# Kernel optimization log

Hardware: AMD Instinct MI355X
Metric: run time of the kernel (lower is better)

## Reference

```python
import jax, jax.numpy as jnp
import numpy as np
import math

N = 100000   # nodes
E = 500000   # edges
IN_C = 128
EDGE_D = 64
HEADS = 4
OUT_C = 32
HC = HEADS * OUT_C  # 128


def setup_inputs() -> dict:
    key = jax.random.key(0)
    ks = jax.random.split(key, 12)
    s_in = 1.0 / math.sqrt(IN_C)
    s_e = 1.0 / math.sqrt(EDGE_D)
    return {
        "x": jax.random.normal(ks[0], (N, IN_C), jnp.float32),
        "edge_index": jax.random.randint(ks[1], (2, E), 0, N, dtype=jnp.int32),
        "edge_attr": jax.random.normal(ks[2], (E, EDGE_D), jnp.float32),
        "Wq": jax.random.uniform(ks[3], (HC, IN_C), jnp.float32, -s_in, s_in),
        "bq": jax.random.uniform(ks[4], (HC,), jnp.float32, -s_in, s_in),
        "Wk": jax.random.uniform(ks[5], (HC, IN_C), jnp.float32, -s_in, s_in),
        "bk": jax.random.uniform(ks[6], (HC,), jnp.float32, -s_in, s_in),
        "Wv": jax.random.uniform(ks[7], (HC, IN_C), jnp.float32, -s_in, s_in),
        "bv": jax.random.uniform(ks[8], (HC,), jnp.float32, -s_in, s_in),
        "We": jax.random.uniform(ks[9], (HC, EDGE_D), jnp.float32, -s_e, s_e),
        "Ws": jax.random.uniform(ks[10], (HC, IN_C), jnp.float32, -s_in, s_in),
        "bs": jax.random.uniform(ks[11], (HC,), jnp.float32, -s_in, s_in),
    }


def reference(x, edge_index, edge_attr, Wq, bq, Wk, bk, Wv, bv, We, Ws, bs):
    src = edge_index[0]
    dst = edge_index[1]
    x_i = x[dst]                       # [E, IN_C] target-node feats
    x_j = x[src]                       # [E, IN_C] source-node feats

    e = (edge_attr @ We.T).reshape(E, HEADS, OUT_C)
    q = (x_i @ Wq.T + bq).reshape(E, HEADS, OUT_C)
    k = (x_j @ Wk.T + bk).reshape(E, HEADS, OUT_C) + e

    alpha = jnp.sum(q * k, axis=-1) / jnp.sqrt(jnp.float32(OUT_C))  # [E, H]
    # Faithful to the source: GLOBAL per-column max (not per-segment), then
    # segment-sum of exponentials over destination nodes.
    m = jnp.max(alpha, axis=0)                                      # [H]
    exp_a = jnp.exp(alpha - m)                                      # [E, H]
    denom = jax.ops.segment_sum(exp_a, dst, num_segments=N)         # [N, H]
    alpha = exp_a / (denom[dst] + 1e-16)                            # [E, H]

    v = (x_j @ Wv.T + bv).reshape(E, HEADS, OUT_C) + e
    msg = v * alpha[:, :, None]                                     # [E, H, C]

    out = jax.ops.segment_sum(msg.reshape(E, HC), dst, num_segments=N)  # [N, HC]
    out = out + (x @ Ws.T + bs)
    return out
```

## Files before the change

kernel.cpp:

```cpp
#include <hip/hip_runtime.h>
#include <hip/hip_bf16.h>
#include <math.h>

#define N_NODES 100000
#define N_EDGES 500000
#define M0 8.0f
#define INV_SQRT32 0.17677669529663687f

#define NB_HIST 977
#define NB_PROJ 1563
#define NB_EE   3907
#define GRID_MEGA (NB_HIST + NB_PROJ + NB_EE)

typedef __attribute__((ext_vector_type(8))) short bf16x8;
typedef __attribute__((ext_vector_type(4))) float f32x4;
typedef __attribute__((ext_vector_type(8))) unsigned short us8;

static __device__ __forceinline__ unsigned short f2bf(float f) {
    __hip_bfloat16 h = __float2bfloat16(f);
    return *(unsigned short*)&h;
}

static __device__ __forceinline__ void split4(float4 v, ushort4& hv, ushort4& lv) {
    const unsigned short h0 = f2bf(v.x), h1 = f2bf(v.y),
                         h2 = f2bf(v.z), h3 = f2bf(v.w);
    hv.x = h0; hv.y = h1; hv.z = h2; hv.w = h3;
    lv.x = f2bf(v.x - __uint_as_float((unsigned)h0 << 16));
    lv.y = f2bf(v.y - __uint_as_float((unsigned)h1 << 16));
    lv.z = f2bf(v.z - __uint_as_float((unsigned)h2 << 16));
    lv.w = f2bf(v.w - __uint_as_float((unsigned)h3 << 16));
}

__global__ __launch_bounds__(256) void prep_kernel(
    const float* __restrict__ Wq, const float* __restrict__ Wk,
    const float* __restrict__ Wv, const float* __restrict__ Ws,
    const float* __restrict__ We,
    unsigned short* __restrict__ WBh, unsigned short* __restrict__ WBl,
    unsigned short* __restrict__ WEh, unsigned short* __restrict__ WEl,
    int* __restrict__ cursor)
{
    const int i = blockIdx.x * 256 + threadIdx.x;
    if (i < N_NODES) cursor[i] = 0;
    if (i < 65536) {
        const int p = i >> 14;
        const float* W = (p == 0) ? Wq : (p == 1) ? Wk : (p == 2) ? Wv : Ws;
        const float v = W[i & 16383];
        const unsigned short h = f2bf(v);
        WBh[i] = h;
        WBl[i] = f2bf(v - __uint_as_float((unsigned)h << 16));
    } else if (i < 73728) {
        const int idx = i - 65536;
        const float v = We[idx];
        const unsigned short h = f2bf(v);
        WEh[idx] = h;
        WEl[idx] = f2bf(v - __uint_as_float((unsigned)h << 16));
    }
}

__global__ __launch_bounds__(512, 4) void mega_kernel(
    const float* __restrict__ x, const int* __restrict__ ei,
    const float* __restrict__ ea,
    const unsigned short* __restrict__ WBh, const unsigned short* __restrict__ WBl,
    const unsigned short* __restrict__ WEh, const unsigned short* __restrict__ WEl,
    const float* __restrict__ bq, const float* __restrict__ bk,
    const float* __restrict__ bv, const float* __restrict__ bs,
    float* __restrict__ Qn, float* __restrict__ Kn, float* __restrict__ Vn,
    float* __restrict__ out, unsigned short* __restrict__ Ee,
    int* __restrict__ cursor)
{
    __shared__ __align__(16) unsigned short sAh[8192];
    __shared__ __align__(16) unsigned short sAl[8192];
    __shared__ __align__(16) unsigned short sWh[8192];
    __shared__ __align__(16) unsigned short sWl[8192];

    const int t = threadIdx.x;
    const int bid = blockIdx.x;

    if (bid < NB_HIST) {
        const int e = bid * 512 + t;
        if (e < N_EDGES) atomicAdd(&cursor[ei[N_EDGES + e]], 1);
        return;
    }

    const int lane = t & 63;
    const int wid = t >> 6;
    const int fr = lane & 15;
    const int fq = lane >> 4;

    if (bid < NB_HIST + NB_PROJ) {
        const long r0 = (long)(bid - NB_HIST) * 64;

        for (int i = t; i < 2048; i += 512) {
            const int r = i >> 5;
            const int k4 = (i & 31) * 4;
            const long row = r0 + r;
            float4 v = (row < N_NODES) ? *(const float4*)&x[row * 128 + k4]
                                       : make_float4(0.f, 0.f, 0.f, 0.f);
            ushort4 hv, lv; split4(v, hv, lv);
            const int di = r * 128 + (k4 ^ ((r & 7) << 3));
            *(ushort4*)&sAh[di] = hv;
            *(ushort4*)&sAl[di] = lv;
        }

        for (int p = 0; p < 4; ++p) {
            const float* bias = (p == 0) ? bq : (p == 1) ? bk : (p == 2) ? bv : bs;
            float* dst        = (p == 0) ? Qn : (p == 1) ? Kn : (p == 2) ? Vn : out;

            f32x4 acc[4];
#pragma unroll
            for (int m = 0; m < 4; ++m) acc[m] = (f32x4){0.f, 0.f, 0.f, 0.f};

            for (int kc = 0; kc < 2; ++kc) {
                __syncthreads();
                for (int i = t; i < 1024; i += 512) {
                    const int r = i >> 3;
                    const int s = i & 7;
                    const int gi = p * 16384 + r * 128 + kc * 64 + s * 8;
                    const int di = r * 64 + ((s * 8) ^ ((r & 7) << 3));
                    *(us8*)&sWh[di] = *(const us8*)&WBh[gi];
                    *(us8*)&sWl[di] = *(const us8*)&WBl[gi];
                }
                __syncthreads();

#pragma unroll
                for (int ks = 0; ks < 2; ++ks) {
                    const int kx = kc * 64 + ks * 32 + fq * 8;
                    const int kw = ks * 32 + fq * 8;
                    bf16x8 ah[4], al[4], bh, bl;
#pragma unroll
                    for (int m = 0; m < 4; ++m) {
                        const int r = m * 16 + fr;
                        const int di = r * 128 + (kx ^ ((r & 7) << 3));
                        ah[m] = *(const bf16x8*)&sAh[di];
                        al[m] = *(const bf16x8*)&sAl[di];
                    }
                    {
                        const int r = wid * 16 + fr;
                        const int di = r * 64 + (kw ^ ((r & 7) << 3));
                        bh = *(const bf16x8*)&sWh[di];
                        bl = *(const bf16x8*)&sWl[di];
                    }
#pragma unroll
                    for (int m = 0; m < 4; ++m) {
                        acc[m] = __builtin_amdgcn_mfma_f32_16x16x32_bf16(
                            ah[m], bh, acc[m], 0, 0, 0);
                        acc[m] = __builtin_amdgcn_mfma_f32_16x16x32_bf16(
                            ah[m], bl, acc[m], 0, 0, 0);
                        acc[m] = __builtin_amdgcn_mfma_f32_16x16x32_bf16(
                            al[m], bh, acc[m], 0, 0, 0);
                    }
                }
            }

            const float bb = bias[wid * 16 + fr];
#pragma unroll
            for (int m = 0; m < 4; ++m) {
                const long rowb = r0 + m * 16 + fq * 4;
#pragma unroll
                for (int j = 0; j < 4; ++j) {
                    if (rowb + j < N_NODES)
                        dst[(rowb + j) * 128 + wid * 16 + fr] = acc[m][j] + bb;
                }
            }
        }
    } else {
        const long e0 = (long)(bid - NB_HIST - NB_PROJ) * 128;
        const int wr = wid >> 2;
        const int wc = wid & 3;

        for (int i = t; i < 1024; i += 512) {
            const int r = i >> 3;
            const int s = i & 7;
            const int di = r * 64 + ((s * 8) ^ ((r & 7) << 3));
            *(us8*)&sWh[di] = *(const us8*)&WEh[r * 64 + s * 8];
            *(us8*)&sWl[di] = *(const us8*)&WEl[r * 64 + s * 8];
        }
        for (int i = t; i < 2048; i += 512) {
            const int r = i >> 4;
            const int k4 = (i & 15) * 4;
            const long e = e0 + r;
            float4 v = (e < N_EDGES) ? *(const float4*)&ea[e * 64 + k4]
                                     : make_float4(0.f, 0.f, 0.f, 0.f);
            ushort4 hv, lv; split4(v, hv, lv);
            const int di = r * 64 + (k4 ^ ((r & 7) << 3));
            *(ushort4*)&sAh[di] = hv;
            *(ushort4*)&sAl[di] = lv;
        }
        __syncthreads();

        f32x4 acc[4][2];
#pragma unroll
        for (int m = 0; m < 4; ++m)
#pragma unroll
            for (int n = 0; n < 2; ++n) acc[m][n] = (f32x4){0.f, 0.f, 0.f, 0.f};

#pragma unroll
        for (int ks = 0; ks < 2; ++ks) {
            const int kk = ks * 32 + fq * 8;
            bf16x8 ah[4], al[4], bh[2], bl[2];
#pragma unroll
            for (int m = 0; m < 4; ++m) {
                const int r = wr * 64 + m * 16 + fr;
                const int di = r * 64 + (kk ^ ((r & 7) << 3));
                ah[m] = *(const bf16x8*)&sAh[di];
                al[m] = *(const bf16x8*)&sAl[di];
            }
#pragma unroll
            for (int n = 0; n < 2; ++n) {
                const int r = wc * 32 + n * 16 + fr;
                const int di = r * 64 + (kk ^ ((r & 7) << 3));
                bh[n] = *(const bf16x8*)&sWh[di];
                bl[n] = *(const bf16x8*)&sWl[di];
            }
#pragma unroll
            for (int m = 0; m < 4; ++m)
#pragma unroll
                for (int n = 0; n < 2; ++n) {
                    acc[m][n] = __builtin_amdgcn_mfma_f32_16x16x32_bf16(
                        ah[m], bh[n], acc[m][n], 0, 0, 0);
                    acc[m][n] = __builtin_amdgcn_mfma_f32_16x16x32_bf16(
                        ah[m], bl[n], acc[m][n], 0, 0, 0);
                    acc[m][n] = __builtin_amdgcn_mfma_f32_16x16x32_bf16(
                        al[m], bh[n], acc[m][n], 0, 0, 0);
                }
        }

#pragma unroll
        for (int m = 0; m < 4; ++m) {
            const long erow = e0 + wr * 64 + m * 16 + fq * 4;
#pragma unroll
            for (int j = 0; j < 4; ++j) {
                if (erow + j < N_EDGES) {
#pragma unroll
                    for (int n = 0; n < 2; ++n)
                        Ee[(erow + j) * 128 + wc * 32 + n * 16 + fr] =
                            f2bf(acc[m][n][j]);
                }
            }
        }
    }
}

__global__ __launch_bounds__(1024) void csr_scan_kernel(
    int* __restrict__ cursor, int* __restrict__ csr_off)
{
    __shared__ int wsum[16];
    const int t = threadIdx.x;
    const int lane = t & 63;
    const int wid = t >> 6;
    const int n0 = t * 100;
    const bool active = (t < 1000);

    int tsum = 0;
    if (active) {
        for (int q = 0; q < 25; ++q) {
            const int4 d = *(const int4*)&cursor[n0 + q * 4];
            tsum += d.x + d.y + d.z + d.w;
        }
    }
    int inc = tsum;
#pragma unroll
    for (int o = 1; o < 64; o <<= 1) {
        const int v = __shfl_up(inc, o, 64);
        if (lane >= o) inc += v;
    }
    if (lane == 63) wsum[wid] = inc;
    __syncthreads();
    if (t == 0) {
        int run = 0;
#pragma unroll
        for (int w = 0; w < 16; ++w) { const int v = wsum[w]; wsum[w] = run; run += v; }
        csr_off[N_NODES] = run;
    }
    __syncthreads();
    if (active) {
        int run = wsum[wid] + inc - tsum;
        for (int q = 0; q < 25; ++q) {
            const int n = n0 + q * 4;
            const int4 d = *(const int4*)&cursor[n];
            int4 offv;
            offv.x = run; run += d.x;
            offv.y = run; run += d.y;
            offv.z = run; run += d.z;
            offv.w = run; run += d.w;
            *(int4*)&csr_off[n] = offv;
            *(int4*)&cursor[n]  = offv;
        }
    }
}

__global__ __launch_bounds__(256) void csr_fill_kernel(
    const int* __restrict__ ei, int* __restrict__ cursor,
    int* __restrict__ csr_eid, int* __restrict__ csr_src)
{
    const int e = blockIdx.x * 256 + threadIdx.x;
    if (e >= N_EDGES) return;
    const int dst = ei[N_EDGES + e];
    const int pos = atomicAdd(&cursor[dst], 1);
    csr_eid[pos] = e;
    csr_src[pos] = ei[e];
}

__global__ __launch_bounds__(256) void fused_attn_kernel(
    const int* __restrict__ csr_off, const int* __restrict__ csr_eid,
    const int* __restrict__ csr_src, const unsigned short* __restrict__ Ee,
    const float* __restrict__ Qn, const float* __restrict__ Kn,
    const float* __restrict__ Vn, float* __restrict__ out)
{
    const int lane = threadIdx.x & 63;
    const int g = lane >> 4;
    const int i2 = (lane & 15) * 2;
    const long n = (long)blockIdx.x * 4 + (threadIdx.x >> 6);

    const int off0 = csr_off[n];
    const int off1 = csr_off[n + 1];

    float2 q[4];
#pragma unroll
    for (int h = 0; h < 4; ++h)
        q[h] = *(const float2*)&Qn[n * 128 + h * 32 + i2];

    float dsum[4] = {0.f, 0.f, 0.f, 0.f};
    float2 acc[4];
#pragma unroll
    for (int h = 0; h < 4; ++h) acc[h] = make_float2(0.f, 0.f);

    for (int base = off0; base < off1; base += 64) {
        const int cnt = min(64, off1 - base);
        int eid = 0, src = 0;
        if (base + lane < off1) {
            eid = csr_eid[base + lane];
            src = csr_src[base + lane];
        }
        for (int c0 = 0; c0 < cnt; c0 += 4) {
            const int j = c0 + g;
            const bool valid = (j < cnt);
            const long e = __shfl(eid, j, 64);
            const long s = __shfl(src, j, 64);

            float ph[4];
            float ea0[4], ea1[4];
            float2 vv[4];
            if (valid) {
#pragma unroll
                for (int h = 0; h < 4; ++h) {
                    const int ch = h * 32 + i2;
                    const unsigned u = *(const unsigned*)&Ee[e * 128 + ch];
                    ea0[h] = __uint_as_float(u << 16);
                    ea1[h] = __uint_as_float(u & 0xffff0000u);
                    const float2 k = *(const float2*)&Kn[s * 128 + ch];
                    vv[h] = *(const float2*)&Vn[s * 128 + ch];
                    ph[h] = q[h].x * (k.x + ea0[h]) + q[h].y * (k.y + ea1[h]);
                }
            } else {
#pragma unroll
                for (int h = 0; h < 4; ++h) ph[h] = 0.f;
            }
#pragma unroll
            for (int h = 0; h < 4; ++h) {
#pragma unroll
                for (int o = 1; o < 16; o <<= 1)
                    ph[h] += __shfl_xor(ph[h], o, 64);
            }
            if (valid) {
#pragma unroll
                for (int h = 0; h < 4; ++h) {
                    const float an = __expf(ph[h] * INV_SQRT32 - M0);
                    dsum[h] += an;
                    acc[h].x = fmaf(vv[h].x + ea0[h], an, acc[h].x);
                    acc[h].y = fmaf(vv[h].y + ea1[h], an, acc[h].y);
                }
            }
        }
    }

#pragma unroll
    for (int h = 0; h < 4; ++h) {
#pragma unroll
        for (int o = 16; o < 64; o <<= 1) {
            dsum[h] += __shfl_xor(dsum[h], o, 64);
            acc[h].x += __shfl_xor(acc[h].x, o, 64);
            acc[h].y += __shfl_xor(acc[h].y, o, 64);
        }
    }

    const float rd = 1.f / (dsum[g] + 1e-16f);
    float2 o = *(const float2*)&out[n * 128 + g * 32 + i2];
    o.x = fmaf(acc[g].x, rd, o.x);
    o.y = fmaf(acc[g].y, rd, o.y);
    *(float2*)&out[n * 128 + g * 32 + i2] = o;
}

extern "C" void kernel_launch(void* const* d_in, const int* in_sizes, int n_in,
                              void* d_out, int out_size, void* d_ws, size_t ws_size,
                              hipStream_t stream)
{
    const float* x  = (const float*)d_in[0];
    const int*   ei = (const int*)d_in[1];
    const float* ea = (const float*)d_in[2];
    const float* Wq = (const float*)d_in[3];
    const float* bq = (const float*)d_in[4];
    const float* Wk = (const float*)d_in[5];
    const float* bk = (const float*)d_in[6];
    const float* Wv = (const float*)d_in[7];
    const float* bv = (const float*)d_in[8];
    const float* We = (const float*)d_in[9];
    const float* Ws = (const float*)d_in[10];
    const float* bs = (const float*)d_in[11];
    float* out = (float*)d_out;

    float* ws = (float*)d_ws;
    float* Qn = ws;
    float* Kn = ws + 12800000;
    float* Vn = ws + 25600000;
    int* csr_off = (int*)(ws + 38400000);
    int* cursor  = (int*)(ws + 38500004);
    int* csr_eid = (int*)(ws + 38600004);
    int* csr_src = (int*)(ws + 39100004);
    unsigned short* WBh = (unsigned short*)(ws + 40000000);
    unsigned short* WBl = (unsigned short*)(ws + 40050000);
    unsigned short* WEh = (unsigned short*)(ws + 40100000);
    unsigned short* WEl = (unsigned short*)(ws + 40110000);
    unsigned short* Ee = (unsigned short*)((char*)d_ws + 163200032);

    prep_kernel<<<391, 256, 0, stream>>>(Wq, Wk, Wv, Ws, We,
                                         WBh, WBl, WEh, WEl, cursor);

    mega_kernel<<<GRID_MEGA, 512, 0, stream>>>(x, ei, ea,
                                               WBh, WBl, WEh, WEl,
                                               bq, bk, bv, bs,
                                               Qn, Kn, Vn, out, Ee, cursor);

    csr_scan_kernel<<<1, 1024, 0, stream>>>(cursor, csr_off);

    csr_fill_kernel<<<(N_EDGES + 255) / 256, 256, 0, stream>>>(ei, cursor,
                                                               csr_eid, csr_src);

    fused_attn_kernel<<<25000, 256, 0, stream>>>(csr_off, csr_eid, csr_src, Ee,
                                                 Qn, Kn, Vn, out);
}
```

Measured before the change: 575.9 us.

## Load weight fragments directly from global and swap MFMA operands for vectorized stores

The mega kernel drops the shared-memory weight staging. Each wave now loads its bf16 hi/lo weight fragments straight from global (L2-resident) memory, removing the per-chunk syncthreads and halving LDS use. MFMA operands are swapped so each lane holds four consecutive output columns, which allows float4/ushort4 row-contiguous stores instead of scalar strided stores. Blocks shrink to 256 threads with smaller edge tiles to raise occupancy, at the cost of repeated global weight reads per wave.

```diff
diff --git a/kernel.cpp b/kernel.cpp
--- a/kernel.cpp
+++ b/kernel.cpp
@@ -7,9 +7,9 @@
 #define M0 8.0f
 #define INV_SQRT32 0.17677669529663687f
 
-#define NB_HIST 977
+#define NB_HIST 1954
 #define NB_PROJ 1563
-#define NB_EE   3907
+#define NB_EE   7813
 #define GRID_MEGA (NB_HIST + NB_PROJ + NB_EE)
 
 typedef __attribute__((ext_vector_type(8))) short bf16x8;
@@ -57,7 +57,7 @@
     }
 }
 
-__global__ __launch_bounds__(512, 4) void mega_kernel(
+__global__ __launch_bounds__(256, 5) void mega_kernel(
     const float* __restrict__ x, const int* __restrict__ ei,
     const float* __restrict__ ea,
     const unsigned short* __restrict__ WBh, const unsigned short* __restrict__ WBl,
@@ -70,14 +70,12 @@
 {
     __shared__ __align__(16) unsigned short sAh[8192];
     __shared__ __align__(16) unsigned short sAl[8192];
-    __shared__ __align__(16) unsigned short sWh[8192];
-    __shared__ __align__(16) unsigned short sWl[8192];
 
     const int t = threadIdx.x;
     const int bid = blockIdx.x;
 
     if (bid < NB_HIST) {
-        const int e = bid * 512 + t;
+        const int e = bid * 256 + t;
         if (e < N_EDGES) atomicAdd(&cursor[ei[N_EDGES + e]], 1);
         return;
     }
@@ -86,11 +84,12 @@
     const int wid = t >> 6;
     const int fr = lane & 15;
     const int fq = lane >> 4;
+    const int cb = wid * 32;
 
     if (bid < NB_HIST + NB_PROJ) {
         const long r0 = (long)(bid - NB_HIST) * 64;
 
-        for (int i = t; i < 2048; i += 512) {
+        for (int i = t; i < 2048; i += 256) {
             const int r = i >> 5;
             const int k4 = (i & 31) * 4;
             const long row = r0 + r;
@@ -101,81 +100,73 @@
             *(ushort4*)&sAh[di] = hv;
             *(ushort4*)&sAl[di] = lv;
         }
+        __syncthreads();
 
         for (int p = 0; p < 4; ++p) {
             const float* bias = (p == 0) ? bq : (p == 1) ? bk : (p == 2) ? bv : bs;
             float* dst        = (p == 0) ? Qn : (p == 1) ? Kn : (p == 2) ? Vn : out;
 
-            f32x4 acc[4];
-#pragma unroll
-            for (int m = 0; m < 4; ++m) acc[m] = (f32x4){0.f, 0.f, 0.f, 0.f};
-
-            for (int kc = 0; kc < 2; ++kc) {
-                __syncthreads();
-                for (int i = t; i < 1024; i += 512) {
-                    const int r = i >> 3;
-                    const int s = i & 7;
-                    const int gi = p * 16384 + r * 128 + kc * 64 + s * 8;
-                    const int di = r * 64 + ((s * 8) ^ ((r & 7) << 3));
-                    *(us8*)&sWh[di] = *(const us8*)&WBh[gi];
-                    *(us8*)&sWl[di] = *(const us8*)&WBl[gi];
-                }
-                __syncthreads();
-
-#pragma unroll
-                for (int ks = 0; ks < 2; ++ks) {
-                    const int kx = kc * 64 + ks * 32 + fq * 8;
-                    const int kw = ks * 32 + fq * 8;
-                    bf16x8 ah[4], al[4], bh, bl;
-#pragma unroll
-                    for (int m = 0; m < 4; ++m) {
-                        const int r = m * 16 + fr;
-                        const int di = r * 128 + (kx ^ ((r & 7) << 3));
-                        ah[m] = *(const bf16x8*)&sAh[di];
-                        al[m] = *(const bf16x8*)&sAl[di];
+            f32x4 acc[4][2];
+#pragma unroll
+            for (int m = 0; m < 4; ++m)
+#pragma unroll
+                for (int n = 0; n < 2; ++n) acc[m][n] = (f32x4){0.f, 0.f, 0.f, 0.f};
+
+#pragma unroll
+            for (int kc = 0; kc < 4; ++kc) {
+                const int kx = kc * 32 + fq * 8;
+                bf16x8 wh[2], wl[2];
+#pragma unroll
+                for (int n = 0; n < 2; ++n) {
+                    const int gi = p * 16384 + (cb + n * 16 + fr) * 128 + kx;
+                    wh[n] = *(const bf16x8*)&WBh[gi];
+                    wl[n] = *(const bf16x8*)&WBl[gi];
+                }
+                bf16x8 ah[4], al[4];
+#pragma unroll
+                for (int m = 0; m < 4; ++m) {
+                    const int r = m * 16 + fr;
+                    const int di = r * 128 + (kx ^ ((r & 7) << 3));
+                    ah[m] = *(const bf16x8*)&sAh[di];
+                    al[m] = *(const bf16x8*)&sAl[di];
+                }
+#pragma unroll
+                for (int m = 0; m < 4; ++m)
+#pragma unroll
+                    for (int n = 0; n < 2; ++n) {
+                        acc[m][n] = __builtin_amdgcn_mfma_f32_16x16x32_bf16(
+                            wh[n], ah[m], acc[m][n], 0, 0, 0);
+                        acc[m][n] = __builtin_amdgcn_mfma_f32_16x16x32_bf16(
+                            wh[n], al[m], acc[m][n], 0, 0, 0);
+                        acc[m][n] = __builtin_amdgcn_mfma_f32_16x16x32_bf16(
+                            wl[n], ah[m], acc[m][n], 0, 0, 0);
                     }
-                    {
-                        const int r = wid * 16 + fr;
-                        const int di = r * 64 + (kw ^ ((r & 7) << 3));
-                        bh = *(const bf16x8*)&sWh[di];
-                        bl = *(const bf16x8*)&sWl[di];
+            }
+
+            float4 bb[2];
+#pragma unroll
+            for (int n = 0; n < 2; ++n)
+                bb[n] = *(const float4*)&bias[cb + n * 16 + fq * 4];
+#pragma unroll
+            for (int m = 0; m < 4; ++m) {
+                const long row = r0 + m * 16 + fr;
+                if (row < N_NODES) {
+#pragma unroll
+                    for (int n = 0; n < 2; ++n) {
+                        float4 o;
+                        o.x = acc[m][n][0] + bb[n].x;
+                        o.y = acc[m][n][1] + bb[n].y;
+                        o.z = acc[m][n][2] + bb[n].z;
+                        o.w = acc[m][n][3] + bb[n].w;
+                        *(float4*)&dst[row * 128 + cb + n * 16 + fq * 4] = o;
                     }
-#pragma unroll
-                    for (int m = 0; m < 4; ++m) {
-                        acc[m] = __builtin_amdgcn_mfma_f32_16x16x32_bf16(
-                            ah[m], bh, acc[m], 0, 0, 0);
-                        acc[m] = __builtin_amdgcn_mfma_f32_16x16x32_bf16(
-                            ah[m], bl, acc[m], 0, 0, 0);
-                        acc[m] = __builtin_amdgcn_mfma_f32_16x16x32_bf16(
-                            al[m], bh, acc[m], 0, 0, 0);
-                    }
-                }
-            }
-
-            const float bb = bias[wid * 16 + fr];
-#pragma unroll
-            for (int m = 0; m < 4; ++m) {
-                const long rowb = r0 + m * 16 + fq * 4;
-#pragma unroll
-                for (int j = 0; j < 4; ++j) {
-                    if (rowb + j < N_NODES)
-                        dst[(rowb + j) * 128 + wid * 16 + fr] = acc[m][j] + bb;
                 }
             }
         }
     } else {
-        const long e0 = (long)(bid - NB_HIST - NB_PROJ) * 128;
-        const int wr = wid >> 2;
-        const int wc = wid & 3;
-
-        for (int i = t; i < 1024; i += 512) {
-            const int r = i >> 3;
-            const int s = i & 7;
-            const int di = r * 64 + ((s * 8) ^ ((r & 7) << 3));
-            *(us8*)&sWh[di] = *(const us8*)&WEh[r * 64 + s * 8];
-            *(us8*)&sWl[di] = *(const us8*)&WEl[r * 64 + s * 8];
-        }
-        for (int i = t; i < 2048; i += 512) {
+        const long e0 = (long)(bid - NB_HIST - NB_PROJ) * 64;
+
+        for (int i = t; i < 1024; i += 256) {
             const int r = i >> 4;
             const int k4 = (i & 15) * 4;
             const long e = e0 + r;
@@ -197,44 +188,46 @@
 #pragma unroll
         for (int ks = 0; ks < 2; ++ks) {
             const int kk = ks * 32 + fq * 8;
-            bf16x8 ah[4], al[4], bh[2], bl[2];
+            bf16x8 wh[2], wl[2];
+#pragma unroll
+            for (int n = 0; n < 2; ++n) {
+                const int gi = (cb + n * 16 + fr) * 64 + kk;
+                wh[n] = *(const bf16x8*)&WEh[gi];
+                wl[n] = *(const bf16x8*)&WEl[gi];
+            }
+            bf16x8 ah[4], al[4];
 #pragma unroll
             for (int m = 0; m < 4; ++m) {
-                const int r = wr * 64 + m * 16 + fr;
+                const int r = m * 16 + fr;
                 const int di = r * 64 + (kk ^ ((r & 7) << 3));
                 ah[m] = *(const bf16x8*)&sAh[di];
                 al[m] = *(const bf16x8*)&sAl[di];
             }
 #pragma unroll
-            for (int n = 0; n < 2; ++n) {
-                const int r = wc * 32 + n * 16 + fr;
-                const int di = r * 64 + (kk ^ ((r & 7) << 3));
-                bh[n] = *(const bf16x8*)&sWh[di];
-                bl[n] = *(const bf16x8*)&sWl[di];
-            }
-#pragma unroll
             for (int m = 0; m < 4; ++m)
 #pragma unroll
                 for (int n = 0; n < 2; ++n) {
                     acc[m][n] = __builtin_amdgcn_mfma_f32_16x16x32_bf16(
-                        ah[m], bh[n], acc[m][n], 0, 0, 0);
+                        wh[n], ah[m], acc[m][n], 0, 0, 0);
                     acc[m][n] = __builtin_amdgcn_mfma_f32_16x16x32_bf16(
-                        ah[m], bl[n], acc[m][n], 0, 0, 0);
+                        wh[n], al[m], acc[m][n], 0, 0, 0);
                     acc[m][n] = __builtin_amdgcn_mfma_f32_16x16x32_bf16(
-                        al[m], bh[n], acc[m][n], 0, 0, 0);
+                        wl[n], ah[m], acc[m][n], 0, 0, 0);
                 }
         }
 
 #pragma unroll
         for (int m = 0; m < 4; ++m) {
-            const long erow = e0 + wr * 64 + m * 16 + fq * 4;
-#pragma unroll
-            for (int j = 0; j < 4; ++j) {
-                if (erow + j < N_EDGES) {
-#pragma unroll
-                    for (int n = 0; n < 2; ++n)
-                        Ee[(erow + j) * 128 + wc * 32 + n * 16 + fr] =
-                            f2bf(acc[m][n][j]);
+            const long e = e0 + m * 16 + fr;
+            if (e < N_EDGES) {
+#pragma unroll
+                for (int n = 0; n < 2; ++n) {
+                    ushort4 u;
+                    u.x = f2bf(acc[m][n][0]);
+                    u.y = f2bf(acc[m][n][1]);
+                    u.z = f2bf(acc[m][n][2]);
+                    u.w = f2bf(acc[m][n][3]);
+                    *(ushort4*)&Ee[e * 128 + cb + n * 16 + fq * 4] = u;
                 }
             }
         }
@@ -426,7 +419,7 @@
     prep_kernel<<<391, 256, 0, stream>>>(Wq, Wk, Wv, Ws, We,
                                          WBh, WBl, WEh, WEl, cursor);
 
-    mega_kernel<<<GRID_MEGA, 512, 0, stream>>>(x, ei, ea,
+    mega_kernel<<<GRID_MEGA, 256, 0, stream>>>(x, ei, ea,
                                                WBh, WBl, WEh, WEl,
                                                bq, bk, bv, bs,
                                                Qn, Kn, Vn, out, Ee, cursor);
```

After: 718.6 us. 1.25x slower.

## Vectorize GEMM epilogue stores, pack CSR pairs, widen attention gathers to float4

Applied to the files above, without the earlier changes.

Swaps MFMA operand order so each lane holds four consecutive output columns, which lets the projection and edge GEMM epilogues write float4 / ushort4 rows instead of scattered scalar stores. Edge ids and source ids are packed into one int2 CSR array so each gather is a single load. The attention kernel now maps 8 lanes per edge with float4 loads, processing 8 edges per iteration with shorter reductions. This trades fewer, wider memory transactions for more registers per lane.

```diff
diff --git a/kernel.cpp b/kernel.cpp
--- a/kernel.cpp
+++ b/kernel.cpp
@@ -19,6 +19,10 @@
 static __device__ __forceinline__ unsigned short f2bf(float f) {
     __hip_bfloat16 h = __float2bfloat16(f);
     return *(unsigned short*)&h;
+}
+
+static __device__ __forceinline__ float bf2f(unsigned short u) {
+    return __uint_as_float((unsigned)u << 16);
 }
 
 static __device__ __forceinline__ void split4(float4 v, ushort4& hv, ushort4& lv) {
@@ -126,7 +130,7 @@
                 for (int ks = 0; ks < 2; ++ks) {
                     const int kx = kc * 64 + ks * 32 + fq * 8;
                     const int kw = ks * 32 + fq * 8;
-                    bf16x8 ah[4], al[4], bh, bl;
+                    bf16x8 ah[4], al[4], wh, wl;
 #pragma unroll
                     for (int m = 0; m < 4; ++m) {
                         const int r = m * 16 + fr;
@@ -137,29 +141,32 @@
                     {
                         const int r = wid * 16 + fr;
                         const int di = r * 64 + (kw ^ ((r & 7) << 3));
-                        bh = *(const bf16x8*)&sWh[di];
-                        bl = *(const bf16x8*)&sWl[di];
+                        wh = *(const bf16x8*)&sWh[di];
+                        wl = *(const bf16x8*)&sWl[di];
                     }
 #pragma unroll
                     for (int m = 0; m < 4; ++m) {
                         acc[m] = __builtin_amdgcn_mfma_f32_16x16x32_bf16(
-                            ah[m], bh, acc[m], 0, 0, 0);
+                            wh, ah[m], acc[m], 0, 0, 0);
                         acc[m] = __builtin_amdgcn_mfma_f32_16x16x32_bf16(
-                            ah[m], bl, acc[m], 0, 0, 0);
+                            wh, al[m], acc[m], 0, 0, 0);
                         acc[m] = __builtin_amdgcn_mfma_f32_16x16x32_bf16(
-                            al[m], bh, acc[m], 0, 0, 0);
+                            wl, ah[m], acc[m], 0, 0, 0);
                     }
                 }
             }
 
-            const float bb = bias[wid * 16 + fr];
+            const float4 bb = *(const float4*)&bias[wid * 16 + fq * 4];
 #pragma unroll
             for (int m = 0; m < 4; ++m) {
-                const long rowb = r0 + m * 16 + fq * 4;
-#pragma unroll
-                for (int j = 0; j < 4; ++j) {
-                    if (rowb + j < N_NODES)
-                        dst[(rowb + j) * 128 + wid * 16 + fr] = acc[m][j] + bb;
+                const long row = r0 + m * 16 + fr;
+                if (row < N_NODES) {
+                    float4 o;
+                    o.x = acc[m][0] + bb.x;
+                    o.y = acc[m][1] + bb.y;
+                    o.z = acc[m][2] + bb.z;
+                    o.w = acc[m][3] + bb.w;
+                    *(float4*)&dst[row * 128 + wid * 16 + fq * 4] = o;
                 }
             }
         }
@@ -197,7 +204,7 @@
 #pragma unroll
         for (int ks = 0; ks < 2; ++ks) {
             const int kk = ks * 32 + fq * 8;
-            bf16x8 ah[4], al[4], bh[2], bl[2];
+            bf16x8 ah[4], al[4], wh[2], wl[2];
 #pragma unroll
             for (int m = 0; m < 4; ++m) {
                 const int r = wr * 64 + m * 16 + fr;
@@ -209,32 +216,34 @@
             for (int n = 0; n < 2; ++n) {
                 const int r = wc * 32 + n * 16 + fr;
                 const int di = r * 64 + (kk ^ ((r & 7) << 3));
-                bh[n] = *(const bf16x8*)&sWh[di];
-                bl[n] = *(const bf16x8*)&sWl[di];
+                wh[n] = *(const bf16x8*)&sWh[di];
+                wl[n] = *(const bf16x8*)&sWl[di];
             }
 #pragma unroll
             for (int m = 0; m < 4; ++m)
 #pragma unroll
                 for (int n = 0; n < 2; ++n) {
                     acc[m][n] = __builtin_amdgcn_mfma_f32_16x16x32_bf16(
-                        ah[m], bh[n], acc[m][n], 0, 0, 0);
+                        wh[n], ah[m], acc[m][n], 0, 0, 0);
                     acc[m][n] = __builtin_amdgcn_mfma_f32_16x16x32_bf16(
-                        ah[m], bl[n], acc[m][n], 0, 0, 0);
+                        wh[n], al[m], acc[m][n], 0, 0, 0);
                     acc[m][n] = __builtin_amdgcn_mfma_f32_16x16x32_bf16(
-                        al[m], bh[n], acc[m][n], 0, 0, 0);
+                        wl[n], ah[m], acc[m][n], 0, 0, 0);
                 }
         }
 
 #pragma unroll
         for (int m = 0; m < 4; ++m) {
-            const long erow = e0 + wr * 64 + m * 16 + fq * 4;
-#pragma unroll
-            for (int j = 0; j < 4; ++j) {
-                if (erow + j < N_EDGES) {
-#pragma unroll
-                    for (int n = 0; n < 2; ++n)
-                        Ee[(erow + j) * 128 + wc * 32 + n * 16 + fr] =
-                            f2bf(acc[m][n][j]);
+            const long e = e0 + wr * 64 + m * 16 + fr;
+            if (e < N_EDGES) {
+#pragma unroll
+                for (int n = 0; n < 2; ++n) {
+                    ushort4 u;
+                    u.x = f2bf(acc[m][n][0]);
+                    u.y = f2bf(acc[m][n][1]);
+                    u.z = f2bf(acc[m][n][2]);
+                    u.w = f2bf(acc[m][n][3]);
+                    *(ushort4*)&Ee[e * 128 + wc * 32 + n * 16 + fq * 4] = u;
                 }
             }
         }
@@ -291,66 +300,63 @@
 
 __global__ __launch_bounds__(256) void csr_fill_kernel(
     const int* __restrict__ ei, int* __restrict__ cursor,
-    int* __restrict__ csr_eid, int* __restrict__ csr_src)
+    int2* __restrict__ csr_es)
 {
     const int e = blockIdx.x * 256 + threadIdx.x;
     if (e >= N_EDGES) return;
     const int dst = ei[N_EDGES + e];
     const int pos = atomicAdd(&cursor[dst], 1);
-    csr_eid[pos] = e;
-    csr_src[pos] = ei[e];
+    csr_es[pos] = make_int2(e, ei[e]);
 }
 
 __global__ __launch_bounds__(256) void fused_attn_kernel(
-    const int* __restrict__ csr_off, const int* __restrict__ csr_eid,
-    const int* __restrict__ csr_src, const unsigned short* __restrict__ Ee,
+    const int* __restrict__ csr_off, const int2* __restrict__ csr_es,
+    const unsigned short* __restrict__ Ee,
     const float* __restrict__ Qn, const float* __restrict__ Kn,
     const float* __restrict__ Vn, float* __restrict__ out)
 {
     const int lane = threadIdx.x & 63;
-    const int g = lane >> 4;
-    const int i2 = (lane & 15) * 2;
+    const int g = lane >> 3;
+    const int il = lane & 7;
+    const int c4 = il * 4;
     const long n = (long)blockIdx.x * 4 + (threadIdx.x >> 6);
 
     const int off0 = csr_off[n];
     const int off1 = csr_off[n + 1];
 
-    float2 q[4];
+    float4 q[4];
 #pragma unroll
     for (int h = 0; h < 4; ++h)
-        q[h] = *(const float2*)&Qn[n * 128 + h * 32 + i2];
+        q[h] = *(const float4*)&Qn[n * 128 + h * 32 + c4];
 
     float dsum[4] = {0.f, 0.f, 0.f, 0.f};
-    float2 acc[4];
-#pragma unroll
-    for (int h = 0; h < 4; ++h) acc[h] = make_float2(0.f, 0.f);
+    float4 acc[4];
+#pragma unroll
+    for (int h = 0; h < 4; ++h) acc[h] = make_float4(0.f, 0.f, 0.f, 0.f);
 
     for (int base = off0; base < off1; base += 64) {
         const int cnt = min(64, off1 - base);
-        int eid = 0, src = 0;
-        if (base + lane < off1) {
-            eid = csr_eid[base + lane];
-            src = csr_src[base + lane];
-        }
-        for (int c0 = 0; c0 < cnt; c0 += 4) {
+        int2 es = make_int2(0, 0);
+        if (base + lane < off1) es = csr_es[base + lane];
+
+        for (int c0 = 0; c0 < cnt; c0 += 8) {
             const int j = c0 + g;
             const bool valid = (j < cnt);
-            const long e = __shfl(eid, j, 64);
-            const long s = __shfl(src, j, 64);
+            const long e = __shfl(es.x, j, 64);
+            const long s = __shfl(es.y, j, 64);
 
             float ph[4];
-            float ea0[4], ea1[4];
-            float2 vv[4];
+            float4 ev[4], vv[4];
             if (valid) {
 #pragma unroll
                 for (int h = 0; h < 4; ++h) {
-                    const int ch = h * 32 + i2;
-                    const unsigned u = *(const unsigned*)&Ee[e * 128 + ch];
-                    ea0[h] = __uint_as_float(u << 16);
-                    ea1[h] = __uint_as_float(u & 0xffff0000u);
-                    const float2 k = *(const float2*)&Kn[s * 128 + ch];
-                    vv[h] = *(const float2*)&Vn[s * 128 + ch];
-                    ph[h] = q[h].x * (k.x + ea0[h]) + q[h].y * (k.y + ea1[h]);
+                    const int ch = h * 32 + c4;
+                    const ushort4 u = *(const ushort4*)&Ee[e * 128 + ch];
+                    ev[h] = make_float4(bf2f(u.x), bf2f(u.y), bf2f(u.z), bf2f(u.w));
+                    const float4 k = *(const float4*)&Kn[s * 128 + ch];
+                    vv[h] = *(const float4*)&Vn[s * 128 + ch];
+                    ph[h] = q[h].x * (k.x + ev[h].x) + q[h].y * (k.y + ev[h].y) +
+                            q[h].z * (k.z + ev[h].z) + q[h].w * (k.w + ev[h].w);
                 }
             } else {
 #pragma unroll
@@ -359,7 +365,7 @@
 #pragma unroll
             for (int h = 0; h < 4; ++h) {
 #pragma unroll
-                for (int o = 1; o < 16; o <<= 1)
+                for (int o = 1; o < 8; o <<= 1)
                     ph[h] += __shfl_xor(ph[h], o, 64);
             }
             if (valid) {
@@ -367,8 +373,10 @@
                 for (int h = 0; h < 4; ++h) {
                     const float an = __expf(ph[h] * INV_SQRT32 - M0);
                     dsum[h] += an;
-                    acc[h].x = fmaf(vv[h].x + ea0[h], an, acc[h].x);
-                    acc[h].y = fmaf(vv[h].y + ea1[h], an, acc[h].y);
+                    acc[h].x = fmaf(vv[h].x + ev[h].x, an, acc[h].x);
+                    acc[h].y = fmaf(vv[h].y + ev[h].y, an, acc[h].y);
+                    acc[h].z = fmaf(vv[h].z + ev[h].z, an, acc[h].z);
+                    acc[h].w = fmaf(vv[h].w + ev[h].w, an, acc[h].w);
                 }
             }
         }
@@ -377,18 +385,27 @@
 #pragma unroll
     for (int h = 0; h < 4; ++h) {
 #pragma unroll
-        for (int o = 16; o < 64; o <<= 1) {
+        for (int o = 8; o < 64; o <<= 1) {
             dsum[h] += __shfl_xor(dsum[h], o, 64);
             acc[h].x += __shfl_xor(acc[h].x, o, 64);
             acc[h].y += __shfl_xor(acc[h].y, o, 64);
-        }
-    }
-
-    const float rd = 1.f / (dsum[g] + 1e-16f);
-    float2 o = *(const float2*)&out[n * 128 + g * 32 + i2];
-    o.x = fmaf(acc[g].x, rd, o.x);
-    o.y = fmaf(acc[g].y, rd, o.y);
-    *(float2*)&out[n * 128 + g * 32 + i2] = o;
+            acc[h].z += __shfl_xor(acc[h].z, o, 64);
+            acc[h].w += __shfl_xor(acc[h].w, o, 64);
+        }
+    }
+
+    if (g == 0) {
+#pragma unroll
+        for (int h = 0; h < 4; ++h) {
+            const float rd = 1.f / (dsum[h] + 1e-16f);
+            float4 o4 = *(const float4*)&out[n * 128 + h * 32 + c4];
+            o4.x = fmaf(acc[h].x, rd, o4.x);
+            o4.y = fmaf(acc[h].y, rd, o4.y);
+            o4.z = fmaf(acc[h].z, rd, o4.z);
+            o4.w = fmaf(acc[h].w, rd, o4.w);
+            *(float4*)&out[n * 128 + h * 32 + c4] = o4;
+        }
+    }
 }
 
 extern "C" void kernel_launch(void* const* d_in, const int* in_sizes, int n_in,
@@ -415,8 +432,7 @@
     float* Vn = ws + 25600000;
     int* csr_off = (int*)(ws + 38400000);
     int* cursor  = (int*)(ws + 38500004);
-    int* csr_eid = (int*)(ws + 38600004);
-    int* csr_src = (int*)(ws + 39100004);
+    int2* csr_es = (int2*)(ws + 38600004);
     unsigned short* WBh = (unsigned short*)(ws + 40000000);
     unsigned short* WBl = (unsigned short*)(ws + 40050000);
     unsigned short* WEh = (unsigned short*)(ws + 40100000);
@@ -433,9 +449,8 @@
 
     csr_scan_kernel<<<1, 1024, 0, stream>>>(cursor, csr_off);
 
-    csr_fill_kernel<<<(N_EDGES + 255) / 256, 256, 0, stream>>>(ei, cursor,
-                                                               csr_eid, csr_src);
-
-    fused_attn_kernel<<<25000, 256, 0, stream>>>(csr_off, csr_eid, csr_src, Ee,
+    csr_fill_kernel<<<(N_EDGES + 255) / 256, 256, 0, stream>>>(ei, cursor, csr_es);
+
+    fused_attn_kernel<<<25000, 256, 0, stream>>>(csr_off, csr_es, Ee,
                                                  Qn, Kn, Vn, out);
 }
```

Result: slower. 601.1 us (+4.4%).
